# Performance work log

Measured on AMD Instinct MI355X. Metric: run time of the kernel, lower is better.

The kernel has to match this reference:

```python
import jax, jax.numpy as jnp
import numpy as np

B, N, C, H = 8, 1024, 768, 12
HEAD_DIM = C // H
EPS = 1e-6


def setup_inputs() -> dict:
    key = jax.random.key(0)
    k1, k2, k3, k4, k5 = jax.random.split(key, 5)
    x = jax.random.normal(k1, (B, N, C), dtype=jnp.float32)
    # binary keep-mask per token, shape (B, N, 1)
    policy = (jax.random.uniform(k2, (B, N, 1)) > 0.3).astype(jnp.float32)
    Wqkv = jax.random.normal(k3, (3 * C, C), dtype=jnp.float32) * 0.02
    Wproj = jax.random.normal(k4, (C, C), dtype=jnp.float32) * 0.02
    bproj = jax.random.normal(k5, (C,), dtype=jnp.float32) * 0.02
    return {"x": x, "policy": policy, "Wqkv": Wqkv, "Wproj": Wproj, "bproj": bproj}


def softmax_with_policy(attn, policy, eps=EPS):
    # attn: (B,H,N,N), policy: (B,N,1) in {0,1}
    Bb, _, Nn, _ = attn.shape
    ap1 = policy.reshape(Bb, 1, 1, Nn)          # key mask
    ap2 = policy.reshape(Bb, 1, Nn, 1)          # query mask
    eye = jnp.eye(Nn, dtype=policy.dtype)[None, None]
    attn_policy = ap1 * ap2 + (1.0 - ap1) * eye  # (B,1,N,N)
    max_att = jnp.max(attn, axis=-1, keepdims=True)
    a = jnp.exp(attn - max_att).astype(jnp.float32) * attn_policy.astype(jnp.float32)
    a = (a + eps / Nn) / (jnp.sum(a, axis=-1, keepdims=True) + eps)
    return a.astype(attn.dtype)


def reference(x, policy, Wqkv, Wproj, bproj):
    Bb, Nn, Cc = x.shape
    scale = HEAD_DIM ** -0.5
    qkv = (x @ Wqkv.T).reshape(Bb, Nn, 3, H, HEAD_DIM).transpose(2, 0, 3, 1, 4)
    q, k, v = qkv[0], qkv[1], qkv[2]            # each (B,H,N,hd)
    attn = jnp.einsum('bhnd,bhmd->bhnm', q, k) * scale
    attn = softmax_with_policy(attn, policy)
    out = jnp.einsum('bhnm,bhmd->bhnd', attn, v)  # (B,H,N,hd)
    out = out.transpose(0, 2, 1, 3).reshape(Bb, Nn, Cc)
    return out @ Wproj.T + bproj
```

## Files before the change

### kernel.cpp

```cpp
#include <hip/hip_runtime.h>
#include <hip/hip_bf16.h>
#include <stdint.h>

#define Bdim 8
#define Nseq 1024
#define Cdim 768
#define Hn 12
#define HD 64
#define EPSf 1e-6f

typedef __bf16 bf16;
typedef __bf16 bf16x8 __attribute__((ext_vector_type(8)));
typedef float f32x4 __attribute__((ext_vector_type(4)));

static __device__ __forceinline__ void gload_lds16(const bf16* g, bf16* lds) {
  __builtin_amdgcn_global_load_lds(
      (const __attribute__((address_space(1))) uint32_t*)g,
      (__attribute__((address_space(3))) uint32_t*)lds, 16, 0, 0);
}

#define NX (Bdim * Nseq * Cdim)
#define NWQ (3 * Cdim * Cdim)
#define NWP (Cdim * Cdim)
__global__ __launch_bounds__(256) void cvt_all(
    const float* __restrict__ x, const float* __restrict__ wq, const float* __restrict__ wp,
    bf16* __restrict__ Xb, bf16* __restrict__ Wqb, bf16* __restrict__ Wpb) {
  const int i = (blockIdx.x * 256 + threadIdx.x) * 8;
  const float* src;
  bf16* dst;
  int off;
  if (i < NX) { src = x; dst = Xb; off = i; }
  else if (i < NX + NWQ) { src = wq; dst = Wqb; off = i - NX; }
  else { src = wp; dst = Wpb; off = i - NX - NWQ; }
  float4 a = *(const float4*)(src + off);
  float4 b = *(const float4*)(src + off + 4);
  bf16x8 o;
  o[0] = (bf16)a.x; o[1] = (bf16)a.y; o[2] = (bf16)a.z; o[3] = (bf16)a.w;
  o[4] = (bf16)b.x; o[5] = (bf16)b.y; o[6] = (bf16)b.z; o[7] = (bf16)b.w;
  *(bf16x8*)(dst + off) = o;
}

__global__ __launch_bounds__(256) void gemm_qkv(
    const bf16* __restrict__ X, const bf16* __restrict__ W,
    bf16* __restrict__ Qb, bf16* __restrict__ Kb, bf16* __restrict__ Vt) {
  __shared__ __align__(16) bf16 As[128 * 32];
  __shared__ __align__(16) bf16 Bs[128 * 32];
  const int t = threadIdx.x;
  const int lane = t & 63;
  const int w = t >> 6;
  const int l15 = lane & 15, quad = lane >> 4;
  const int wm = w & 1, wn = w >> 1;
  const int mbase = blockIdx.y * 128;
  const int nbase = blockIdx.x * 128;
  constexpr int K = Cdim;

  const int srow = t >> 2;
  const int scol = (t & 3) * 8;
  const bf16* Ag = X + (size_t)(mbase + srow) * K + scol;
  const bf16* Bg = W + (size_t)(nbase + srow) * K + scol;
  bf16* AsT = As + t * 8;
  bf16* BsT = Bs + t * 8;

  f32x4 acc[4][4] = {};

  for (int kt = 0; kt < K; kt += 32) {
    gload_lds16(Ag + kt, AsT);
    gload_lds16(Ag + (size_t)64 * K + kt, AsT + 2048);
    gload_lds16(Bg + kt, BsT);
    gload_lds16(Bg + (size_t)64 * K + kt, BsT + 2048);
    __syncthreads();
    bf16x8 a[4], b[4];
#pragma unroll
    for (int mt = 0; mt < 4; mt++)
      a[mt] = *(const bf16x8*)(As + (wm * 64 + mt * 16 + l15) * 32 + quad * 8);
#pragma unroll
    for (int nt = 0; nt < 4; nt++)
      b[nt] = *(const bf16x8*)(Bs + (wn * 64 + nt * 16 + l15) * 32 + quad * 8);
#pragma unroll
    for (int mt = 0; mt < 4; mt++)
#pragma unroll
      for (int nt = 0; nt < 4; nt++)
        acc[mt][nt] = __builtin_amdgcn_mfma_f32_16x16x32_bf16(a[mt], b[nt], acc[mt][nt], 0, 0, 0);
    __syncthreads();
  }

  const int s = nbase / Cdim;
  const float oscale = (s == 0) ? 0.125f : 1.0f;
  const int jbase = (nbase % Cdim) + wn * 64;
#pragma unroll
  for (int nt = 0; nt < 4; nt++) {
    const int jj = jbase + nt * 16 + l15;
    const int h = jj >> 6, d = jj & 63;
#pragma unroll
    for (int mt = 0; mt < 4; mt++) {
#pragma unroll
      for (int r = 0; r < 4; r++) {
        const int m = mbase + wm * 64 + mt * 16 + quad * 4 + r;
        const int b_ = m >> 10, n = m & 1023;
        const bf16 v = (bf16)(acc[mt][nt][r] * oscale);
        const size_t bh = (size_t)b_ * Hn + h;
        if (s == 0)      Qb[(bh * Nseq + n) * HD + d] = v;
        else if (s == 1) Kb[(bh * Nseq + n) * HD + d] = v;
        else             Vt[(bh * HD + d) * Nseq + n] = v;
      }
    }
  }
}

__global__ __launch_bounds__(256) void colsum_v(const bf16* __restrict__ Vt,
                                                float* __restrict__ CS) {
  const int row = blockIdx.x * 4 + (threadIdx.x >> 6);
  const int lane = threadIdx.x & 63;
  const bf16x8* p = (const bf16x8*)(Vt + (size_t)row * Nseq + lane * 16);
  bf16x8 v0 = p[0], v1 = p[1];
  float s = 0.f;
#pragma unroll
  for (int i = 0; i < 8; i++) s += (float)v0[i] + (float)v1[i];
#pragma unroll
  for (int off = 1; off < 64; off <<= 1) s += __shfl_xor(s, off);
  if (lane == 0) CS[row] = s;
}

template <bool DIAG>
static __device__ __forceinline__ void smax_update(
    f32x4 (&S)[2][4], float (&mx)[2][4], float (&lrow)[2][4],
    const float (&polq)[2][4], const float (&polk)[4],
    int kt, int qbase, int quad, int l15) {
#pragma unroll
  for (int u = 0; u < 2; u++)
#pragma unroll
    for (int r = 0; r < 4; r++) {
      const float pm = polq[u][r];
      const float m4 = fmaxf(fmaxf(S[u][0][r], S[u][1][r]), fmaxf(S[u][2][r], S[u][3][r]));
      mx[u][r] = fmaxf(mx[u][r], m4);
      const int q = qbase + u * 16 + quad * 4 + r;
      float psum = 0.f;
#pragma unroll
      for (int s = 0; s < 4; s++) {
        const float e = __expf(S[u][s][r]);
        float p = e * (polk[s] * pm);
        if (DIAG) p = (q == kt + s * 16 + l15) ? e : p;
        S[u][s][r] = p;
        psum += p;
      }
      lrow[u][r] += psum;
    }
}

__global__ __launch_bounds__(256) void attn_fused(
    const bf16* __restrict__ Qb, const bf16* __restrict__ Kb, const bf16* __restrict__ Vt,
    const float* __restrict__ pol, const float* __restrict__ CS, bf16* __restrict__ O) {
  __shared__ __align__(16) bf16 Ks[64 * 64];
  __shared__ __align__(16) bf16 Vs[64 * 64];
  __shared__ __align__(16) bf16 Pbuf[4][32 * 40];
  __shared__ float Ps[Nseq];
  const int t = threadIdx.x, w = t >> 6, lane = t & 63;
  const int l15 = lane & 15, quad = lane >> 4;

  const int bx = blockIdx.x;
  const int g = (bx & 7) + 8 * (bx >> 6);
  const int qt = (bx >> 3) & 7;
  const int b_ = g / Hn, h = g % Hn;
  const int qbase = qt * 128 + w * 32;
  const int ktdiag = qbase & ~63;

  const bf16* Qp = Qb + (size_t)g * Nseq * HD;
  const bf16* Kp = Kb + (size_t)g * Nseq * HD;
  const bf16* Vp = Vt + (size_t)g * HD * Nseq;
  const float* polb = pol + (size_t)b_ * Nseq;

  *(float4*)(Ps + t * 4) = *(const float4*)(polb + t * 4);

  const int ci0 = t, ci1 = t + 256;
  const int row0 = ci0 >> 3, seg0 = (ci0 & 7) ^ (row0 & 7);
  const int row1 = ci1 >> 3, seg1 = (ci1 & 7) ^ (row1 & 7);

  bf16x8 aq[2][2];
#pragma unroll
  for (int u = 0; u < 2; u++) {
    aq[u][0] = *(const bf16x8*)(Qp + (qbase + u * 16 + l15) * HD + quad * 8);
    aq[u][1] = *(const bf16x8*)(Qp + (qbase + u * 16 + l15) * HD + 32 + quad * 8);
  }

  float polq[2][4];
#pragma unroll
  for (int u = 0; u < 2; u++)
#pragma unroll
    for (int r = 0; r < 4; r++) polq[u][r] = polb[qbase + u * 16 + quad * 4 + r];

  float mx[2][4], lrow[2][4];
  f32x4 oacc[2][4] = {};
#pragma unroll
  for (int u = 0; u < 2; u++)
#pragma unroll
    for (int r = 0; r < 4; r++) { mx[u][r] = -1e30f; lrow[u][r] = 0.f; }

  bf16* Pw = &Pbuf[w][0];
  const int swA = (quad ^ (l15 & 7)) * 8;
  const int swB = ((quad ^ 4) ^ (l15 & 7)) * 8;

  for (int kt = 0; kt < Nseq; kt += 64) {
    __syncthreads();
    gload_lds16(Kp + (kt + row0) * HD + seg0 * 8, Ks + ci0 * 8);
    gload_lds16(Kp + (kt + row1) * HD + seg1 * 8, Ks + ci1 * 8);
    gload_lds16(Vp + (size_t)row0 * Nseq + kt + seg0 * 8, Vs + ci0 * 8);
    gload_lds16(Vp + (size_t)row1 * Nseq + kt + seg1 * 8, Vs + ci1 * 8);
    __syncthreads();

    f32x4 S[2][4] = {};
#pragma unroll
    for (int s = 0; s < 4; s++) {
      const int i = s * 16 + l15;
      bf16x8 bk0 = *(const bf16x8*)(Ks + i * 64 + swA);
      bf16x8 bk1 = *(const bf16x8*)(Ks + i * 64 + swB);
#pragma unroll
      for (int u = 0; u < 2; u++) {
        S[u][s] = __builtin_amdgcn_mfma_f32_16x16x32_bf16(aq[u][0], bk0, S[u][s], 0, 0, 0);
        S[u][s] = __builtin_amdgcn_mfma_f32_16x16x32_bf16(aq[u][1], bk1, S[u][s], 0, 0, 0);
      }
    }

    float polk[4];
#pragma unroll
    for (int s = 0; s < 4; s++) polk[s] = Ps[kt + s * 16 + l15];

    if (kt == ktdiag)
      smax_update<true>(S, mx, lrow, polq, polk, kt, qbase, quad, l15);
    else
      smax_update<false>(S, mx, lrow, polq, polk, kt, qbase, quad, l15);

#pragma unroll
    for (int hh = 0; hh < 2; hh++) {
#pragma unroll
      for (int u = 0; u < 2; u++)
#pragma unroll
        for (int sl = 0; sl < 2; sl++)
#pragma unroll
          for (int r = 0; r < 4; r++)
            Pw[(u * 16 + quad * 4 + r) * 40 + sl * 16 + l15] = (bf16)S[u][hh * 2 + sl][r];
      asm volatile("s_waitcnt lgkmcnt(0)" ::: "memory");
      bf16x8 ap[2];
#pragma unroll
      for (int u = 0; u < 2; u++)
        ap[u] = *(const bf16x8*)(Pw + (u * 16 + l15) * 40 + quad * 8);
      const int swV = (((hh * 4 + quad)) ^ (l15 & 7)) * 8;
#pragma unroll
      for (int c = 0; c < 4; c++) {
        const int i = c * 16 + l15;
        bf16x8 bv = *(const bf16x8*)(Vs + i * 64 + swV);
#pragma unroll
        for (int u = 0; u < 2; u++)
          oacc[u][c] = __builtin_amdgcn_mfma_f32_16x16x32_bf16(ap[u], bv, oacc[u][c], 0, 0, 0);
      }
    }
  }

  float rden[2][4], eterm[2][4];
  const float epsN = EPSf / (float)Nseq;
#pragma unroll
  for (int u = 0; u < 2; u++)
#pragma unroll
    for (int r = 0; r < 4; r++) {
      float v = lrow[u][r];
      v += __shfl_xor(v, 1);
      v += __shfl_xor(v, 2);
      v += __shfl_xor(v, 4);
      v += __shfl_xor(v, 8);
      float m = mx[u][r];
      m = fmaxf(m, __shfl_xor(m, 1));
      m = fmaxf(m, __shfl_xor(m, 2));
      m = fmaxf(m, __shfl_xor(m, 4));
      m = fmaxf(m, __shfl_xor(m, 8));
      const float em = __expf(m);
      rden[u][r] = 1.f / (v + EPSf * em);
      eterm[u][r] = epsN * em;
    }
  const float* CSp = CS + (size_t)g * HD;
#pragma unroll
  for (int c = 0; c < 4; c++) {
    const float cs = CSp[c * 16 + l15];
#pragma unroll
    for (int u = 0; u < 2; u++)
#pragma unroll
      for (int r = 0; r < 4; r++) {
        const int q = qbase + u * 16 + quad * 4 + r;
        const float val = (oacc[u][c][r] + cs * eterm[u][r]) * rden[u][r];
        O[((size_t)b_ * Nseq + q) * Cdim + h * 64 + c * 16 + l15] = (bf16)val;
      }
  }
}

__global__ __launch_bounds__(256) void gemm_proj(
    const bf16* __restrict__ A_, const bf16* __restrict__ W,
    const float* __restrict__ bias, float* __restrict__ out) {
  __shared__ __align__(16) bf16 As[128 * 32];
  __shared__ __align__(16) bf16 Bs[128 * 32];
  const int t = threadIdx.x;
  const int lane = t & 63;
  const int w = t >> 6;
  const int l15 = lane & 15, quad = lane >> 4;
  const int wm = w & 1, wn = w >> 1;
  const int mbase = blockIdx.y * 128;
  const int nbase = blockIdx.x * 128;
  constexpr int K = Cdim;

  const int srow = t >> 2;
  const int scol = (t & 3) * 8;
  const bf16* Ag = A_ + (size_t)(mbase + srow) * K + scol;
  const bf16* Bg = W + (size_t)(nbase + srow) * K + scol;
  bf16* AsT = As + t * 8;
  bf16* BsT = Bs + t * 8;

  f32x4 acc[4][4] = {};

  for (int kt = 0; kt < K; kt += 32) {
    gload_lds16(Ag + kt, AsT);
    gload_lds16(Ag + (size_t)64 * K + kt, AsT + 2048);
    gload_lds16(Bg + kt, BsT);
    gload_lds16(Bg + (size_t)64 * K + kt, BsT + 2048);
    __syncthreads();
    bf16x8 a[4], b[4];
#pragma unroll
    for (int mt = 0; mt < 4; mt++)
      a[mt] = *(const bf16x8*)(As + (wm * 64 + mt * 16 + l15) * 32 + quad * 8);
#pragma unroll
    for (int nt = 0; nt < 4; nt++)
      b[nt] = *(const bf16x8*)(Bs + (wn * 64 + nt * 16 + l15) * 32 + quad * 8);
#pragma unroll
    for (int mt = 0; mt < 4; mt++)
#pragma unroll
      for (int nt = 0; nt < 4; nt++)
        acc[mt][nt] = __builtin_amdgcn_mfma_f32_16x16x32_bf16(a[mt], b[nt], acc[mt][nt], 0, 0, 0);
    __syncthreads();
  }

#pragma unroll
  for (int nt = 0; nt < 4; nt++) {
    const int j = nbase + wn * 64 + nt * 16 + l15;
    const float bj = bias[j];
#pragma unroll
    for (int mt = 0; mt < 4; mt++)
#pragma unroll
      for (int r = 0; r < 4; r++) {
        const int m = mbase + wm * 64 + mt * 16 + quad * 4 + r;
        out[(size_t)m * Cdim + j] = acc[mt][nt][r] + bj;
      }
  }
}

extern "C" void kernel_launch(void* const* d_in, const int* in_sizes, int n_in,
                              void* d_out, int out_size, void* d_ws, size_t ws_size,
                              hipStream_t stream) {
  const float* x = (const float*)d_in[0];
  const float* pol = (const float*)d_in[1];
  const float* Wqkv = (const float*)d_in[2];
  const float* Wproj = (const float*)d_in[3];
  const float* bproj = (const float*)d_in[4];
  float* out = (float*)d_out;
  char* ws = (char*)d_ws;

  const size_t SZ = (size_t)Bdim * Hn * Nseq * HD * sizeof(bf16);
  bf16* Qb = (bf16*)(ws);
  bf16* Kb = (bf16*)(ws + SZ);
  bf16* Vt = (bf16*)(ws + 2 * SZ);
  bf16* O  = (bf16*)(ws + 3 * SZ);
  float* CS = (float*)(ws + 4 * SZ);
  bf16* Xb = (bf16*)(ws + 4 * SZ + 32 * 1024);
  bf16* Wqkvb = Xb + (size_t)Bdim * Nseq * Cdim;
  bf16* Wprojb = Wqkvb + (size_t)3 * Cdim * Cdim;

  cvt_all<<<(NX + NWQ + NWP) / 2048, 256, 0, stream>>>(x, Wqkv, Wproj, Xb, Wqkvb, Wprojb);

  gemm_qkv<<<dim3(3 * Cdim / 128, (Bdim * Nseq) / 128), 256, 0, stream>>>(Xb, Wqkvb, Qb, Kb, Vt);
  colsum_v<<<(Bdim * Hn * HD) / 4, 256, 0, stream>>>(Vt, CS);
  attn_fused<<<Bdim * Hn * (Nseq / 128), 256, 0, stream>>>(Qb, Kb, Vt, pol, CS, O);
  gemm_proj<<<dim3(Cdim / 128, (Bdim * Nseq) / 128), 256, 0, stream>>>(O, Wprojb, bproj, out);
}
```

Before: 240.8 us.

## Fuse V column-sum into QKV GEMM and retile GEMMs with swizzled LDS

Removes the separate colsum_v kernel. The V column sums are now reduced from the QKV GEMM accumulators and added into a buffer that cvt_all zeroes, using atomics. Both GEMMs move to a K-step of 64 with an XOR-swizzled LDS layout to cut bank conflicts, and remap blocks so neighbouring tiles land on the same XCD for L2 locality. The projection GEMM switches to 64x128 tiles to launch more blocks. The cost is float atomics whose summation order is nondeterministic, and larger LDS use per block.

```diff
diff --git a/kernel.cpp b/kernel.cpp
--- a/kernel.cpp
+++ b/kernel.cpp
@@ -24,7 +24,9 @@
 #define NWP (Cdim * Cdim)
 __global__ __launch_bounds__(256) void cvt_all(
     const float* __restrict__ x, const float* __restrict__ wq, const float* __restrict__ wp,
-    bf16* __restrict__ Xb, bf16* __restrict__ Wqb, bf16* __restrict__ Wpb) {
+    bf16* __restrict__ Xb, bf16* __restrict__ Wqb, bf16* __restrict__ Wpb,
+    float* __restrict__ CS) {
+  if (blockIdx.x < 24) CS[blockIdx.x * 256 + threadIdx.x] = 0.f;
   const int i = (blockIdx.x * 256 + threadIdx.x) * 8;
   const float* src;
   bf16* dst;
@@ -42,51 +44,67 @@
 
 __global__ __launch_bounds__(256) void gemm_qkv(
     const bf16* __restrict__ X, const bf16* __restrict__ W,
-    bf16* __restrict__ Qb, bf16* __restrict__ Kb, bf16* __restrict__ Vt) {
-  __shared__ __align__(16) bf16 As[128 * 32];
-  __shared__ __align__(16) bf16 Bs[128 * 32];
+    bf16* __restrict__ Qb, bf16* __restrict__ Kb, bf16* __restrict__ Vt,
+    float* __restrict__ CS) {
+  __shared__ __align__(16) bf16 As[128 * 64];
+  __shared__ __align__(16) bf16 Bs[128 * 64];
   const int t = threadIdx.x;
   const int lane = t & 63;
   const int w = t >> 6;
   const int l15 = lane & 15, quad = lane >> 4;
   const int wm = w & 1, wn = w >> 1;
-  const int mbase = blockIdx.y * 128;
-  const int nbase = blockIdx.x * 128;
   constexpr int K = Cdim;
 
-  const int srow = t >> 2;
-  const int scol = (t & 3) * 8;
-  const bf16* Ag = X + (size_t)(mbase + srow) * K + scol;
-  const bf16* Bg = W + (size_t)(nbase + srow) * K + scol;
-  bf16* AsT = As + t * 8;
-  bf16* BsT = Bs + t * 8;
-
+  const int flat = blockIdx.y * 18 + blockIdx.x;
+  const int xcd = flat & 7, idx = flat >> 3;
+  const int my = (idx & 7) + xcd * 8;
+  const int nx = idx >> 3;
+  const int mbase = my * 128;
+  const int nbase = nx * 128;
+
+  const int srow = t >> 3, slot = t & 7;
   f32x4 acc[4][4] = {};
 
-  for (int kt = 0; kt < K; kt += 32) {
-    gload_lds16(Ag + kt, AsT);
-    gload_lds16(Ag + (size_t)64 * K + kt, AsT + 2048);
-    gload_lds16(Bg + kt, BsT);
-    gload_lds16(Bg + (size_t)64 * K + kt, BsT + 2048);
-    __syncthreads();
-    bf16x8 a[4], b[4];
-#pragma unroll
-    for (int mt = 0; mt < 4; mt++)
-      a[mt] = *(const bf16x8*)(As + (wm * 64 + mt * 16 + l15) * 32 + quad * 8);
-#pragma unroll
-    for (int nt = 0; nt < 4; nt++)
-      b[nt] = *(const bf16x8*)(Bs + (wn * 64 + nt * 16 + l15) * 32 + quad * 8);
-#pragma unroll
-    for (int mt = 0; mt < 4; mt++)
-#pragma unroll
-      for (int nt = 0; nt < 4; nt++)
-        acc[mt][nt] = __builtin_amdgcn_mfma_f32_16x16x32_bf16(a[mt], b[nt], acc[mt][nt], 0, 0, 0);
+  for (int kt = 0; kt < K; kt += 64) {
+#pragma unroll
+    for (int j = 0; j < 4; j++) {
+      const int row = j * 32 + srow;
+      const int seg = slot ^ (row & 7);
+      gload_lds16(X + (size_t)(mbase + row) * K + kt + seg * 8, As + (j * 256 + t) * 8);
+    }
+#pragma unroll
+    for (int j = 0; j < 4; j++) {
+      const int row = j * 32 + srow;
+      const int seg = slot ^ (row & 7);
+      gload_lds16(W + (size_t)(nbase + row) * K + kt + seg * 8, Bs + (j * 256 + t) * 8);
+    }
+    __syncthreads();
+#pragma unroll
+    for (int kh = 0; kh < 2; kh++) {
+      bf16x8 a[4], b[4];
+#pragma unroll
+      for (int mt = 0; mt < 4; mt++) {
+        const int row = wm * 64 + mt * 16 + l15;
+        a[mt] = *(const bf16x8*)(As + row * 64 + ((kh * 4 + quad) ^ (row & 7)) * 8);
+      }
+#pragma unroll
+      for (int nt = 0; nt < 4; nt++) {
+        const int row = wn * 64 + nt * 16 + l15;
+        b[nt] = *(const bf16x8*)(Bs + row * 64 + ((kh * 4 + quad) ^ (row & 7)) * 8);
+      }
+#pragma unroll
+      for (int mt = 0; mt < 4; mt++)
+#pragma unroll
+        for (int nt = 0; nt < 4; nt++)
+          acc[mt][nt] = __builtin_amdgcn_mfma_f32_16x16x32_bf16(a[mt], b[nt], acc[mt][nt], 0, 0, 0);
+    }
     __syncthreads();
   }
 
   const int s = nbase / Cdim;
   const float oscale = (s == 0) ? 0.125f : 1.0f;
   const int jbase = (nbase % Cdim) + wn * 64;
+  const int b0 = mbase >> 10;
 #pragma unroll
   for (int nt = 0; nt < 4; nt++) {
     const int jj = jbase + nt * 16 + l15;
@@ -96,29 +114,31 @@
 #pragma unroll
       for (int r = 0; r < 4; r++) {
         const int m = mbase + wm * 64 + mt * 16 + quad * 4 + r;
-        const int b_ = m >> 10, n = m & 1023;
+        const int n = m & 1023;
         const bf16 v = (bf16)(acc[mt][nt][r] * oscale);
-        const size_t bh = (size_t)b_ * Hn + h;
+        const size_t bh = (size_t)b0 * Hn + h;
         if (s == 0)      Qb[(bh * Nseq + n) * HD + d] = v;
         else if (s == 1) Kb[(bh * Nseq + n) * HD + d] = v;
         else             Vt[(bh * HD + d) * Nseq + n] = v;
       }
     }
   }
-}
-
-__global__ __launch_bounds__(256) void colsum_v(const bf16* __restrict__ Vt,
-                                                float* __restrict__ CS) {
-  const int row = blockIdx.x * 4 + (threadIdx.x >> 6);
-  const int lane = threadIdx.x & 63;
-  const bf16x8* p = (const bf16x8*)(Vt + (size_t)row * Nseq + lane * 16);
-  bf16x8 v0 = p[0], v1 = p[1];
-  float s = 0.f;
-#pragma unroll
-  for (int i = 0; i < 8; i++) s += (float)v0[i] + (float)v1[i];
-#pragma unroll
-  for (int off = 1; off < 64; off <<= 1) s += __shfl_xor(s, off);
-  if (lane == 0) CS[row] = s;
+  if (s == 2) {
+#pragma unroll
+    for (int nt = 0; nt < 4; nt++) {
+      float v = 0.f;
+#pragma unroll
+      for (int mt = 0; mt < 4; mt++)
+#pragma unroll
+        for (int r = 0; r < 4; r++) v += acc[mt][nt][r];
+      v += __shfl_xor(v, 16);
+      v += __shfl_xor(v, 32);
+      if (quad == 0) {
+        const int jj = jbase + nt * 16 + l15;
+        atomicAdd(&CS[((size_t)b0 * Hn + (jj >> 6)) * HD + (jj & 63)], v);
+      }
+    }
+  }
 }
 
 template <bool DIAG>
@@ -293,56 +313,69 @@
 __global__ __launch_bounds__(256) void gemm_proj(
     const bf16* __restrict__ A_, const bf16* __restrict__ W,
     const float* __restrict__ bias, float* __restrict__ out) {
-  __shared__ __align__(16) bf16 As[128 * 32];
-  __shared__ __align__(16) bf16 Bs[128 * 32];
+  __shared__ __align__(16) bf16 As[64 * 64];
+  __shared__ __align__(16) bf16 Bs[128 * 64];
   const int t = threadIdx.x;
   const int lane = t & 63;
-  const int w = t >> 6;
+  const int wn = t >> 6;
   const int l15 = lane & 15, quad = lane >> 4;
-  const int wm = w & 1, wn = w >> 1;
-  const int mbase = blockIdx.y * 128;
-  const int nbase = blockIdx.x * 128;
   constexpr int K = Cdim;
 
-  const int srow = t >> 2;
-  const int scol = (t & 3) * 8;
-  const bf16* Ag = A_ + (size_t)(mbase + srow) * K + scol;
-  const bf16* Bg = W + (size_t)(nbase + srow) * K + scol;
-  bf16* AsT = As + t * 8;
-  bf16* BsT = Bs + t * 8;
-
-  f32x4 acc[4][4] = {};
-
-  for (int kt = 0; kt < K; kt += 32) {
-    gload_lds16(Ag + kt, AsT);
-    gload_lds16(Ag + (size_t)64 * K + kt, AsT + 2048);
-    gload_lds16(Bg + kt, BsT);
-    gload_lds16(Bg + (size_t)64 * K + kt, BsT + 2048);
-    __syncthreads();
-    bf16x8 a[4], b[4];
+  const int flat = blockIdx.y * 6 + blockIdx.x;
+  const int xcd = flat & 7, idx = flat >> 3;
+  const int my = (idx & 15) + xcd * 16;
+  const int nx = idx >> 4;
+  const int mbase = my * 64;
+  const int nbase = nx * 128;
+
+  const int srow = t >> 3, slot = t & 7;
+  f32x4 acc[4][2] = {};
+
+  for (int kt = 0; kt < K; kt += 64) {
+#pragma unroll
+    for (int j = 0; j < 2; j++) {
+      const int row = j * 32 + srow;
+      const int seg = slot ^ (row & 7);
+      gload_lds16(A_ + (size_t)(mbase + row) * K + kt + seg * 8, As + (j * 256 + t) * 8);
+    }
+#pragma unroll
+    for (int j = 0; j < 4; j++) {
+      const int row = j * 32 + srow;
+      const int seg = slot ^ (row & 7);
+      gload_lds16(W + (size_t)(nbase + row) * K + kt + seg * 8, Bs + (j * 256 + t) * 8);
+    }
+    __syncthreads();
+#pragma unroll
+    for (int kh = 0; kh < 2; kh++) {
+      bf16x8 a[4], b[2];
+#pragma unroll
+      for (int mt = 0; mt < 4; mt++) {
+        const int row = mt * 16 + l15;
+        a[mt] = *(const bf16x8*)(As + row * 64 + ((kh * 4 + quad) ^ (row & 7)) * 8);
+      }
+#pragma unroll
+      for (int nt = 0; nt < 2; nt++) {
+        const int row = wn * 32 + nt * 16 + l15;
+        b[nt] = *(const bf16x8*)(Bs + row * 64 + ((kh * 4 + quad) ^ (row & 7)) * 8);
+      }
+#pragma unroll
+      for (int mt = 0; mt < 4; mt++)
+#pragma unroll
+        for (int nt = 0; nt < 2; nt++)
+          acc[mt][nt] = __builtin_amdgcn_mfma_f32_16x16x32_bf16(a[mt], b[nt], acc[mt][nt], 0, 0, 0);
+    }
+    __syncthreads();
+  }
+
+#pragma unroll
+  for (int nt = 0; nt < 2; nt++) {
+    const int j = nbase + wn * 32 + nt * 16 + l15;
+    const float bj = bias[j];
 #pragma unroll
     for (int mt = 0; mt < 4; mt++)
-      a[mt] = *(const bf16x8*)(As + (wm * 64 + mt * 16 + l15) * 32 + quad * 8);
-#pragma unroll
-    for (int nt = 0; nt < 4; nt++)
-      b[nt] = *(const bf16x8*)(Bs + (wn * 64 + nt * 16 + l15) * 32 + quad * 8);
-#pragma unroll
-    for (int mt = 0; mt < 4; mt++)
-#pragma unroll
-      for (int nt = 0; nt < 4; nt++)
-        acc[mt][nt] = __builtin_amdgcn_mfma_f32_16x16x32_bf16(a[mt], b[nt], acc[mt][nt], 0, 0, 0);
-    __syncthreads();
-  }
-
-#pragma unroll
-  for (int nt = 0; nt < 4; nt++) {
-    const int j = nbase + wn * 64 + nt * 16 + l15;
-    const float bj = bias[j];
-#pragma unroll
-    for (int mt = 0; mt < 4; mt++)
 #pragma unroll
       for (int r = 0; r < 4; r++) {
-        const int m = mbase + wm * 64 + mt * 16 + quad * 4 + r;
+        const int m = mbase + mt * 16 + quad * 4 + r;
         out[(size_t)m * Cdim + j] = acc[mt][nt][r] + bj;
       }
   }
@@ -369,10 +402,8 @@
   bf16* Wqkvb = Xb + (size_t)Bdim * Nseq * Cdim;
   bf16* Wprojb = Wqkvb + (size_t)3 * Cdim * Cdim;
 
-  cvt_all<<<(NX + NWQ + NWP) / 2048, 256, 0, stream>>>(x, Wqkv, Wproj, Xb, Wqkvb, Wprojb);
-
-  gemm_qkv<<<dim3(3 * Cdim / 128, (Bdim * Nseq) / 128), 256, 0, stream>>>(Xb, Wqkvb, Qb, Kb, Vt);
-  colsum_v<<<(Bdim * Hn * HD) / 4, 256, 0, stream>>>(Vt, CS);
+  cvt_all<<<(NX + NWQ + NWP) / 2048, 256, 0, stream>>>(x, Wqkv, Wproj, Xb, Wqkvb, Wprojb, CS);
+  gemm_qkv<<<dim3(18, 64), 256, 0, stream>>>(Xb, Wqkvb, Qb, Kb, Vt, CS);
   attn_fused<<<Bdim * Hn * (Nseq / 128), 256, 0, stream>>>(Qb, Kb, Vt, pol, CS, O);
-  gemm_proj<<<dim3(Cdim / 128, (Bdim * Nseq) / 128), 256, 0, stream>>>(O, Wprojb, bproj, out);
-}
+  gemm_proj<<<dim3(6, 128), 256, 0, stream>>>(O, Wprojb, bproj, out);
+}
```

New measurement: 221.8 us. -7.9%, faster.
